# Kernel optimization log

Hardware: AMD Instinct MI355X
Metric: run time of the kernel (lower is better)

The kernel has to match this reference:

```python
import jax, jax.numpy as jnp
import numpy as np

N = 50000      # num nodes
E = 800000     # num edges (before self loops)
DIN = 128      # input_dim
HID = 32       # hidden_dim per head
HEADS = 4
DOUT = 128     # output_dim
NEG_SLOPE = 0.2
EPS = 1e-5


def setup_inputs() -> dict:
    key = jax.random.key(0)
    ks = jax.random.split(key, 16)
    s = 0.05
    return {
        "x": jax.random.normal(ks[0], (N, DIN), dtype=jnp.float32),
        "edge_index": jax.random.randint(ks[1], (2, E), 0, N, dtype=jnp.int64),
        # GAT layer 1 (heads=4, concat=True)
        "W1": jax.random.normal(ks[2], (DIN, HEADS * HID), dtype=jnp.float32) * s,
        "att_src1": jax.random.normal(ks[3], (HEADS, HID), dtype=jnp.float32) * s,
        "att_dst1": jax.random.normal(ks[4], (HEADS, HID), dtype=jnp.float32) * s,
        "b1": jnp.zeros((HEADS * HID,), dtype=jnp.float32),
        # GAT layer 2 (heads=1, concat=False)
        "W2": jax.random.normal(ks[5], (HEADS * HID, DOUT), dtype=jnp.float32) * s,
        "att_src2": jax.random.normal(ks[6], (1, DOUT), dtype=jnp.float32) * s,
        "att_dst2": jax.random.normal(ks[7], (1, DOUT), dtype=jnp.float32) * s,
        "b2": jnp.zeros((DOUT,), dtype=jnp.float32),
        # LayerNorms
        "g1": jnp.ones((HEADS * HID,), dtype=jnp.float32),
        "be1": jnp.zeros((HEADS * HID,), dtype=jnp.float32),
        "g2": jnp.ones((DOUT,), dtype=jnp.float32),
        "be2": jnp.zeros((DOUT,), dtype=jnp.float32),
    }


def gat_conv(x, src, dst, W, a_src, a_dst, n_nodes):
    # x: [N, Fin]; W: [Fin, H*C]; a_src/a_dst: [H, C]
    H, C = a_src.shape
    h = (x @ W).reshape(-1, H, C)                       # [N, H, C]
    es = jnp.einsum("nhc,hc->nh", h, a_src)             # [N, H]
    ed = jnp.einsum("nhc,hc->nh", h, a_dst)             # [N, H]
    e = jax.nn.leaky_relu(es[src] + ed[dst], NEG_SLOPE)  # [E, H]
    # segment softmax over incoming edges of each dst node
    m = jax.ops.segment_max(e, dst, num_segments=n_nodes)
    a = jnp.exp(e - jax.lax.stop_gradient(m)[dst])
    den = jax.ops.segment_sum(a, dst, num_segments=n_nodes)
    alpha = a / den[dst]                                 # [E, H]
    out = jax.ops.segment_sum(alpha[:, :, None] * h[src], dst,
                              num_segments=n_nodes)      # [N, H, C]
    return out


def layer_norm(x, g, b):
    mu = jnp.mean(x, axis=-1, keepdims=True)
    var = jnp.mean((x - mu) ** 2, axis=-1, keepdims=True)
    return (x - mu) * jax.lax.rsqrt(var + EPS) * g + b


def reference(x, edge_index, W1, att_src1, att_dst1, b1,
              W2, att_src2, att_dst2, b2, g1, be1, g2, be2):
    n = x.shape[0]
    loop = jnp.arange(n, dtype=edge_index.dtype)
    src = jnp.concatenate([edge_index[0], loop])  # PyG add_self_loops=True
    dst = jnp.concatenate([edge_index[1], loop])

    h = gat_conv(x, src, dst, W1, att_src1, att_dst1, n)   # [N, 4, 32]
    h = h.reshape(n, -1) + b1                              # concat=True
    h = jax.nn.relu(layer_norm(h, g1, be1))                # dropout = id (eval)

    o = gat_conv(h, src, dst, W2, att_src2, att_dst2, n)   # [N, 1, DOUT]
    o = o[:, 0, :] + b2                                    # concat=False, 1 head
    o = jax.nn.relu(layer_norm(o, g2, be2))
    return o
```

## Files before the change

kernel.cpp:

```cpp
#include <hip/hip_runtime.h>

#define NEG 0.2f
#define LNEPS 1e-5f

static __device__ __forceinline__ float leaky(float e){ return fmaxf(e, NEG*e); }

static __device__ __forceinline__ unsigned pack_bf16(float a, float b){
  unsigned ua = __float_as_uint(a), ub = __float_as_uint(b);
  ua += 0x7FFFu + ((ua>>16)&1u);
  ub += 0x7FFFu + ((ub>>16)&1u);
  return (ua>>16) | (ub & 0xFFFF0000u);
}
static __device__ __forceinline__ float lo_bf(unsigned u){ return __uint_as_float(u<<16); }
static __device__ __forceinline__ float hi_bf(unsigned u){ return __uint_as_float(u & 0xFFFF0000u); }

typedef float f32x4 __attribute__((ext_vector_type(4)));
typedef short s16x8 __attribute__((ext_vector_type(8)));
union U4V8 { uint4 u; s16x8 v; };


__global__ __launch_bounds__(256) void k_bhist(const int* __restrict__ dst, int* __restrict__ bcnt, int E){
  __shared__ int h[256];
  int t = threadIdx.x;
  h[t] = 0; __syncthreads();
  int base = blockIdx.x * 2048;
  int cnt = min(2048, E - base);
  for (int i = t; i < cnt; i += 256) atomicAdd(&h[((unsigned)dst[base+i]) >> 8], 1);
  __syncthreads();
  if (h[t]) atomicAdd(&bcnt[t], h[t]);
}

__global__ __launch_bounds__(256) void k_bscan(const int* __restrict__ bcnt, int* __restrict__ boff,
                                               int* __restrict__ off, int N, int E){
  __shared__ int sm[256];
  int t = threadIdx.x;
  int v = bcnt[t];
  sm[t] = v; __syncthreads();
  for (int o=1;o<256;o<<=1){ int add=(t>=o)?sm[t-o]:0; __syncthreads(); sm[t]+=add; __syncthreads(); }
  boff[t+1] = sm[t];
  if (t==0){ boff[0] = 0; off[N] = E; }
}

__global__ __launch_bounds__(256) void k_bstage(const int* __restrict__ src, const int* __restrict__ dst,
                                                const int* __restrict__ boff, int* __restrict__ bfill,
                                                unsigned* __restrict__ stage, int E){
  __shared__ int h[256];
  __shared__ int sm[256];
  __shared__ int sb[256];
  __shared__ int cur[256];
  __shared__ int rb[256];
  __shared__ unsigned buf[2048];
  int t = threadIdx.x;
  h[t] = 0; __syncthreads();
  int base = blockIdx.x * 2048;
  int cnt = min(2048, E - base);
  for (int i = t; i < cnt; i += 256) atomicAdd(&h[((unsigned)dst[base+i]) >> 8], 1);
  __syncthreads();
  int hv = h[t];
  sm[t] = hv; __syncthreads();
  for (int o=1;o<256;o<<=1){ int add=(t>=o)?sm[t-o]:0; __syncthreads(); sm[t]+=add; __syncthreads(); }
  sb[t] = sm[t] - hv;
  cur[t] = sm[t] - hv;
  rb[t] = (hv > 0) ? atomicAdd(&bfill[t], hv) : 0;
  __syncthreads();
  for (int i = t; i < cnt; i += 256){
    unsigned d = (unsigned)dst[base+i];
    unsigned v = (unsigned)src[base+i] | (d << 16);
    int p = atomicAdd(&cur[d >> 8], 1);
    buf[p] = v;
  }
  __syncthreads();
  for (int i = t; i < cnt; i += 256){
    unsigned v = buf[i];
    int b = v >> 24;
    stage[ (size_t)(boff[b] + rb[b] + (i - sb[b])) ] = v;
  }
}

__global__ __launch_bounds__(1024) void k_bucket(const unsigned* __restrict__ stage, const int* __restrict__ boff,
                                                 int* __restrict__ off, unsigned* __restrict__ csr2, int N){
  __shared__ int cnt[256];
  __shared__ int sm[256];
  __shared__ int cur[256];
  int b = blockIdx.x, t = threadIdx.x;
  int lo = boff[b], hi = boff[b+1];
  if (t < 256) cnt[t] = 0;
  __syncthreads();
  for (int i = lo + t; i < hi; i += 1024) atomicAdd(&cnt[(stage[i] >> 16) & 0xFF], 1);
  __syncthreads();
  if (t < 256){ sm[t] = cnt[t]; }
  __syncthreads();
  for (int o=1;o<256;o<<=1){
    int add = (t < 256 && t >= o) ? sm[t-o] : 0;
    __syncthreads();
    if (t < 256) sm[t] += add;
    __syncthreads();
  }
  if (t < 256){
    int ex = sm[t] - cnt[t];
    cur[t] = ex;
    int d = (b << 8) + t;
    if (d < N) off[d] = lo + ex;
  }
  __syncthreads();
  for (int i = lo + t; i < hi; i += 1024){
    unsigned v = stage[i];
    int p = atomicAdd(&cur[(v >> 16) & 0xFF], 1);
    csr2[(size_t)(lo + p)] = v;
  }
}


__global__ __launch_bounds__(256) void k_wprep(const float* __restrict__ W, uint4* __restrict__ Wb){
  int i = blockIdx.x*256 + threadIdx.x;
  int lane = i & 63, t = (i>>6)&7, k0 = i>>9;
  int c = lane & 15, q = lane >> 4;
  const float* base = &W[(size_t)(k0*32 + q*8)*128 + t*16 + c];
  uint4 u;
  u.x = pack_bf16(base[0*128], base[1*128]);
  u.y = pack_bf16(base[2*128], base[3*128]);
  u.z = pack_bf16(base[4*128], base[5*128]);
  u.w = pack_bf16(base[6*128], base[7*128]);
  Wb[i] = u;
}


template<int HEADS, bool PACKED>
__global__ __launch_bounds__(256) void k_gemm_mfma(const float* __restrict__ A,
                                                   const unsigned* __restrict__ Ab,
                                                   const uint4* __restrict__ Wb,
                                                   const float* __restrict__ as, const float* __restrict__ ad,
                                                   unsigned* __restrict__ Hb, float* __restrict__ es,
                                                   float* __restrict__ ed, float* __restrict__ m0, int n){
  __shared__ unsigned hstage[4][16*68];
  int tid = threadIdx.x;
  int wave = tid >> 6, lane = tid & 63;
  int c = lane & 15, q = lane >> 4;
  int r0 = blockIdx.x*64 + wave*16;
  int rowa = r0 + c;
  int rowc = min(rowa, n-1);
  f32x4 acc[8];
  #pragma unroll
  for (int t=0;t<8;++t) acc[t] = (f32x4){0.f,0.f,0.f,0.f};

  #pragma unroll
  for (int k0 = 0; k0 < 4; ++k0){
    U4V8 af;
    if (PACKED){
      af.u = *(const uint4*)&Ab[(size_t)rowc*64 + k0*16 + q*4];
    } else {
      const float* ap = &A[(size_t)rowc*128 + k0*32 + q*8];
      float4 v0 = *(const float4*)ap;
      float4 v1 = *(const float4*)(ap+4);
      af.u.x = pack_bf16(v0.x, v0.y);
      af.u.y = pack_bf16(v0.z, v0.w);
      af.u.z = pack_bf16(v1.x, v1.y);
      af.u.w = pack_bf16(v1.z, v1.w);
    }
    #pragma unroll
    for (int t=0;t<8;++t){
      U4V8 bf;
      bf.u = Wb[(k0*8+t)*64 + lane];
      acc[t] = __builtin_amdgcn_mfma_f32_16x16x32_bf16(af.v, bf.v, acc[t], 0, 0, 0);
    }
  }

  float asv[8], adv[8];
  #pragma unroll
  for (int t=0;t<8;++t){ asv[t] = as[t*16+c]; adv[t] = ad[t*16+c]; }
  if (HEADS == 4){
    float pes[4][4], ped[4][4];
    #pragma unroll
    for (int r=0;r<4;++r)
      #pragma unroll
      for (int h=0;h<4;++h){ pes[r][h]=0.f; ped[r][h]=0.f; }
    #pragma unroll
    for (int t=0;t<8;++t)
      #pragma unroll
      for (int r=0;r<4;++r){
        pes[r][t>>1] = fmaf(acc[t][r], asv[t], pes[r][t>>1]);
        ped[r][t>>1] = fmaf(acc[t][r], adv[t], ped[r][t>>1]);
      }
    #pragma unroll
    for (int r=0;r<4;++r)
      #pragma unroll
      for (int h=0;h<4;++h){
        #pragma unroll
        for (int m=1;m<16;m<<=1){
          pes[r][h] += __shfl_xor(pes[r][h], m);
          ped[r][h] += __shfl_xor(ped[r][h], m);
        }
      }
    if (c == 0){
      #pragma unroll
      for (int r=0;r<4;++r){
        int row2 = r0 + q*4 + r;
        if (row2 < n){
          float4 e = make_float4(pes[r][0],pes[r][1],pes[r][2],pes[r][3]);
          float4 d = make_float4(ped[r][0],ped[r][1],ped[r][2],ped[r][3]);
          float4 mm = make_float4(leaky(e.x+d.x),leaky(e.y+d.y),leaky(e.z+d.z),leaky(e.w+d.w));
          *(float4*)&es[(size_t)row2*4] = e;
          *(float4*)&ed[(size_t)row2*4] = d;
          *(float4*)&m0[(size_t)row2*4] = mm;
        }
      }
    }
  } else {
    float pes[4] = {0.f,0.f,0.f,0.f}, ped[4] = {0.f,0.f,0.f,0.f};
    #pragma unroll
    for (int t=0;t<8;++t)
      #pragma unroll
      for (int r=0;r<4;++r){
        pes[r] = fmaf(acc[t][r], asv[t], pes[r]);
        ped[r] = fmaf(acc[t][r], adv[t], ped[r]);
      }
    #pragma unroll
    for (int r=0;r<4;++r){
      #pragma unroll
      for (int m=1;m<16;m<<=1){
        pes[r] += __shfl_xor(pes[r], m);
        ped[r] += __shfl_xor(ped[r], m);
      }
    }
    if (c == 0){
      #pragma unroll
      for (int r=0;r<4;++r){
        int row2 = r0 + q*4 + r;
        if (row2 < n){
          es[row2] = pes[r]; ed[row2] = ped[r]; m0[row2] = leaky(pes[r]+ped[r]);
        }
      }
    }
  }

  unsigned* hs = hstage[wave];
  #pragma unroll
  for (int t=0;t<8;++t)
    #pragma unroll
    for (int r=0;r<4;++r){
      float other = __shfl_xor(acc[t][r], 1);
      if (!(c & 1)) hs[(q*4+r)*68 + t*8 + (c>>1)] = pack_bf16(acc[t][r], other);
    }
  #pragma unroll
  for (int it=0; it<4; ++it){
    int idx = it*64 + lane;
    int rr = idx >> 4, c4 = idx & 15;
    int grow = r0 + rr;
    if (grow < n)
      *(uint4*)&Hb[(size_t)grow*64 + c4*4] = *(uint4*)&hs[rr*68 + c4*4];
  }
}


template<bool OUT_PACKED>
__global__ __launch_bounds__(256) void k_agg4(const unsigned* __restrict__ Hb,
                                              const float* __restrict__ es, const float* __restrict__ ed,
                                              const float* __restrict__ m0,
                                              const int* __restrict__ off, const unsigned* __restrict__ csr2,
                                              const float* __restrict__ bias, const float* __restrict__ g,
                                              const float* __restrict__ be, float* __restrict__ out,
                                              unsigned* __restrict__ outp, int N){
  int lane = threadIdx.x & 63;
  int node = blockIdx.x*4 + (threadIdx.x >> 6);
  if (node >= N) return;
  int hh = lane >> 4;
  int wsrc = lane & 48;
  float edn = ed[(size_t)node*4 + hh];
  float m0n = m0[(size_t)node*4 + hh];
  float l = 1.f;
  unsigned uself = Hb[(size_t)node*64 + lane];
  float a1 = lo_bf(uself), a2 = hi_bf(uself);
  int j0 = off[node], j1 = off[node+1];
  for (int c0 = j0; c0 < j1; c0 += 16){
    int m = min(16, j1 - c0);
    int eidx = lane & 15;
    int sv = 0; float wv = 0.f;
    if (eidx < m){
      unsigned v = csr2[c0 + eidx];
      sv = v & 0xFFFF;
      float e = es[(size_t)sv*4 + hh];
      wv = __expf(leaky(e + edn) - m0n);
    }
    int j = 0;
    for (; j+3 < m; j += 4){
      int s0 = __shfl(sv, j), s1 = __shfl(sv, j+1), s2 = __shfl(sv, j+2), s3 = __shfl(sv, j+3);
      float w0 = __shfl(wv, wsrc | j);
      float w1 = __shfl(wv, wsrc | (j+1));
      float w2 = __shfl(wv, wsrc | (j+2));
      float w3 = __shfl(wv, wsrc | (j+3));
      unsigned u0 = Hb[(size_t)s0*64 + lane];
      unsigned u1 = Hb[(size_t)s1*64 + lane];
      unsigned u2 = Hb[(size_t)s2*64 + lane];
      unsigned u3 = Hb[(size_t)s3*64 + lane];
      l += (w0 + w1) + (w2 + w3);
      a1 = fmaf(w0, lo_bf(u0), a1); a2 = fmaf(w0, hi_bf(u0), a2);
      a1 = fmaf(w1, lo_bf(u1), a1); a2 = fmaf(w1, hi_bf(u1), a2);
      a1 = fmaf(w2, lo_bf(u2), a1); a2 = fmaf(w2, hi_bf(u2), a2);
      a1 = fmaf(w3, lo_bf(u3), a1); a2 = fmaf(w3, hi_bf(u3), a2);
    }
    for (; j < m; ++j){
      int s0 = __shfl(sv, j);
      float w0 = __shfl(wv, wsrc | j);
      unsigned u0 = Hb[(size_t)s0*64 + lane];
      l += w0;
      a1 = fmaf(w0, lo_bf(u0), a1); a2 = fmaf(w0, hi_bf(u0), a2);
    }
  }
  float rl = __frcp_rn(l);
  float2 bv = *(const float2*)&bias[2*lane];
  float v1 = a1 * rl + bv.x;
  float v2 = a2 * rl + bv.y;
  float s = v1 + v2;
  #pragma unroll
  for (int m=32;m>0;m>>=1) s += __shfl_xor(s,m);
  float mu = s * (1.f/128.f);
  float d1 = v1-mu, d2 = v2-mu;
  float ss = d1*d1 + d2*d2;
  #pragma unroll
  for (int m=32;m>0;m>>=1) ss += __shfl_xor(ss,m);
  float rs = rsqrtf(ss*(1.f/128.f) + LNEPS);
  float2 gv = *(const float2*)&g[2*lane];
  float2 bev = *(const float2*)&be[2*lane];
  float y1 = fmaxf(d1*rs*gv.x + bev.x, 0.f);
  float y2 = fmaxf(d2*rs*gv.y + bev.y, 0.f);
  if (OUT_PACKED){
    outp[(size_t)node*64 + lane] = pack_bf16(y1, y2);
  } else {
    *(float2*)&out[(size_t)node*128 + 2*lane] = make_float2(y1, y2);
  }
}

__global__ __launch_bounds__(256) void k_agg1(const unsigned* __restrict__ Hb,
                                              const float* __restrict__ es, const float* __restrict__ ed,
                                              const float* __restrict__ m0,
                                              const int* __restrict__ off, const unsigned* __restrict__ csr2,
                                              const float* __restrict__ bias, const float* __restrict__ g,
                                              const float* __restrict__ be, float* __restrict__ out, int N){
  int lane = threadIdx.x & 63;
  int node = blockIdx.x*4 + (threadIdx.x >> 6);
  if (node >= N) return;
  float edn = ed[node];
  float m0n = m0[node];
  float l = 1.f;
  unsigned uself = Hb[(size_t)node*64 + lane];
  float a1 = lo_bf(uself), a2 = hi_bf(uself);
  int j0 = off[node], j1 = off[node+1];
  for (int c0 = j0; c0 < j1; c0 += 64){
    int m = min(64, j1 - c0);
    int sv = 0; float wv = 0.f;
    if (lane < m){
      unsigned v = csr2[c0 + lane];
      sv = v & 0xFFFF;
      wv = __expf(leaky(es[sv] + edn) - m0n);
    }
    int j = 0;
    for (; j+3 < m; j += 4){
      int s0 = __shfl(sv, j), s1 = __shfl(sv, j+1), s2 = __shfl(sv, j+2), s3 = __shfl(sv, j+3);
      float w0 = __shfl(wv, j), w1 = __shfl(wv, j+1), w2 = __shfl(wv, j+2), w3 = __shfl(wv, j+3);
      unsigned u0 = Hb[(size_t)s0*64 + lane];
      unsigned u1 = Hb[(size_t)s1*64 + lane];
      unsigned u2 = Hb[(size_t)s2*64 + lane];
      unsigned u3 = Hb[(size_t)s3*64 + lane];
      l += (w0 + w1) + (w2 + w3);
      a1 = fmaf(w0, lo_bf(u0), a1); a2 = fmaf(w0, hi_bf(u0), a2);
      a1 = fmaf(w1, lo_bf(u1), a1); a2 = fmaf(w1, hi_bf(u1), a2);
      a1 = fmaf(w2, lo_bf(u2), a1); a2 = fmaf(w2, hi_bf(u2), a2);
      a1 = fmaf(w3, lo_bf(u3), a1); a2 = fmaf(w3, hi_bf(u3), a2);
    }
    for (; j < m; ++j){
      int s0 = __shfl(sv, j);
      float w0 = __shfl(wv, j);
      unsigned u0 = Hb[(size_t)s0*64 + lane];
      l += w0;
      a1 = fmaf(w0, lo_bf(u0), a1); a2 = fmaf(w0, hi_bf(u0), a2);
    }
  }
  float rl = __frcp_rn(l);
  float2 bv = *(const float2*)&bias[2*lane];
  float v1 = a1 * rl + bv.x;
  float v2 = a2 * rl + bv.y;
  float s = v1 + v2;
  #pragma unroll
  for (int mm=32;mm>0;mm>>=1) s += __shfl_xor(s,mm);
  float mu = s * (1.f/128.f);
  float d1 = v1-mu, d2 = v2-mu;
  float ss = d1*d1 + d2*d2;
  #pragma unroll
  for (int mm=32;mm>0;mm>>=1) ss += __shfl_xor(ss,mm);
  float rs = rsqrtf(ss*(1.f/128.f) + LNEPS);
  float2 gv = *(const float2*)&g[2*lane];
  float2 bev = *(const float2*)&be[2*lane];
  float y1 = fmaxf(d1*rs*gv.x + bev.x, 0.f);
  float y2 = fmaxf(d2*rs*gv.y + bev.y, 0.f);
  *(float2*)&out[(size_t)node*128 + 2*lane] = make_float2(y1, y2);
}


extern "C" void kernel_launch(void* const* d_in, const int* in_sizes, int n_in,
                              void* d_out, int out_size, void* d_ws, size_t ws_size,
                              hipStream_t stream){
  const float* x   = (const float*)d_in[0];
  const int*   ei  = (const int*)  d_in[1];
  const float* W1  = (const float*)d_in[2];
  const float* as1 = (const float*)d_in[3];
  const float* ad1 = (const float*)d_in[4];
  const float* b1  = (const float*)d_in[5];
  const float* W2  = (const float*)d_in[6];
  const float* as2 = (const float*)d_in[7];
  const float* ad2 = (const float*)d_in[8];
  const float* b2  = (const float*)d_in[9];
  const float* g1  = (const float*)d_in[10];
  const float* be1 = (const float*)d_in[11];
  const float* g2  = (const float*)d_in[12];
  const float* be2 = (const float*)d_in[13];

  int N = in_sizes[0] / 128;
  int E = in_sizes[1] / 2;
  const int* src = ei;
  const int* dst = ei + E;

  char* p = (char*)d_ws;
  auto carve = [&](size_t bytes)->char*{ char* r = p; p += ((bytes + 255) / 256) * 256; return r; };
  unsigned* Hb = (unsigned*)carve((size_t)N*64*4);
  unsigned* Bb = (unsigned*)carve((size_t)N*64*4);
  float* es1 = (float*)carve((size_t)N*4*4);
  float* ed1 = (float*)carve((size_t)N*4*4);
  float* m01 = (float*)carve((size_t)N*4*4);
  float* es2 = (float*)carve((size_t)N*4);
  float* ed2 = (float*)carve((size_t)N*4);
  float* m02 = (float*)carve((size_t)N*4);
  int* off   = (int*)carve((size_t)(N+1)*4);
  unsigned* stg = (unsigned*)carve((size_t)E*4);
  unsigned* csr2= (unsigned*)carve((size_t)E*4);
  uint4* W1b = (uint4*)carve(2048*16);
  uint4* W2b = (uint4*)carve(2048*16);
  int* bcnt  = (int*)carve(256*4);
  int* bfill = (int*)carve(256*4);
  int* boff  = (int*)carve(257*4);

  hipMemsetAsync(bcnt, 0, 256*4, stream);
  hipMemsetAsync(bfill, 0, 256*4, stream);

  int nbe = (E + 2047) / 2048;
  int NB  = (N + 255) >> 8;
  int gb  = (N + 63) / 64;
  int nb4 = (N + 3) / 4;

  k_wprep <<<8, 256, 0, stream>>>(W1, W1b);
  k_wprep <<<8, 256, 0, stream>>>(W2, W2b);
  k_bhist <<<nbe, 256, 0, stream>>>(dst, bcnt, E);
  k_bscan <<<1,   256, 0, stream>>>(bcnt, boff, off, N, E);
  k_bstage<<<nbe, 256, 0, stream>>>(src, dst, boff, bfill, stg, E);
  k_bucket<<<NB, 1024, 0, stream>>>(stg, boff, off, csr2, N);

  k_gemm_mfma<4,false><<<gb, 256, 0, stream>>>(x, nullptr, W1b, as1, ad1, Hb, es1, ed1, m01, N);
  k_agg4<true><<<nb4, 256, 0, stream>>>(Hb, es1, ed1, m01, off, csr2, b1, g1, be1, nullptr, Bb, N);
  k_gemm_mfma<1,true><<<gb, 256, 0, stream>>>(nullptr, Bb, W2b, as2, ad2, Hb, es2, ed2, m02, N);
  k_agg1<<<nb4, 256, 0, stream>>>(Hb, es2, ed2, m02, off, csr2, b2, g2, be2, (float*)d_out, N);
}
```

Measured before the change: 255.0 us.

## Use wave-level scans, merge prep launches and memsets, unroll gathers by eight

Replaces the 256-element barrier-based Hillis-Steele scans in the CSR build kernels with a single-wave shuffle scan. Merges the two weight-prep launches into one and the two counter memsets into one covering both adjacent buffers. Adds an 8-way unrolled gather loop in both aggregation kernels so more independent row loads are in flight. The goal is fewer launches and barriers plus more memory-level parallelism, at the cost of higher register pressure in the aggregation kernels. The merged memset depends on the two counter buffers being laid out back to back.

After: 247.4 us. 1.03x faster.

```diff
diff --git a/kernel.cpp b/kernel.cpp
--- a/kernel.cpp
+++ b/kernel.cpp
@@ -17,6 +17,20 @@
 typedef float f32x4 __attribute__((ext_vector_type(4)));
 typedef short s16x8 __attribute__((ext_vector_type(8)));
 union U4V8 { uint4 u; s16x8 v; };
+
+static __device__ __forceinline__ void wave_scan256(int* sm, int t){
+  if (t < 64){
+    int a0=sm[t*4], a1=sm[t*4+1], a2=sm[t*4+2], a3=sm[t*4+3];
+    int s = a0+a1+a2+a3, sc = s;
+    #pragma unroll
+    for (int o=1;o<64;o<<=1){ int x = __shfl_up(sc, o); if (t >= o) sc += x; }
+    int e = sc - s;
+    sm[t*4]   = e;
+    sm[t*4+1] = e + a0;
+    sm[t*4+2] = e + a0 + a1;
+    sm[t*4+3] = e + a0 + a1 + a2;
+  }
+}
 
 
 __global__ __launch_bounds__(256) void k_bhist(const int* __restrict__ dst, int* __restrict__ bcnt, int E){
@@ -36,8 +50,9 @@
   int t = threadIdx.x;
   int v = bcnt[t];
   sm[t] = v; __syncthreads();
-  for (int o=1;o<256;o<<=1){ int add=(t>=o)?sm[t-o]:0; __syncthreads(); sm[t]+=add; __syncthreads(); }
-  boff[t+1] = sm[t];
+  wave_scan256(sm, t);
+  __syncthreads();
+  boff[t+1] = sm[t] + v;
   if (t==0){ boff[0] = 0; off[N] = E; }
 }
 
@@ -58,9 +73,11 @@
   __syncthreads();
   int hv = h[t];
   sm[t] = hv; __syncthreads();
-  for (int o=1;o<256;o<<=1){ int add=(t>=o)?sm[t-o]:0; __syncthreads(); sm[t]+=add; __syncthreads(); }
-  sb[t] = sm[t] - hv;
-  cur[t] = sm[t] - hv;
+  wave_scan256(sm, t);
+  __syncthreads();
+  int excl = sm[t];
+  sb[t] = excl;
+  cur[t] = excl;
   rb[t] = (hv > 0) ? atomicAdd(&bfill[t], hv) : 0;
   __syncthreads();
   for (int i = t; i < cnt; i += 256){
@@ -88,16 +105,12 @@
   __syncthreads();
   for (int i = lo + t; i < hi; i += 1024) atomicAdd(&cnt[(stage[i] >> 16) & 0xFF], 1);
   __syncthreads();
-  if (t < 256){ sm[t] = cnt[t]; }
-  __syncthreads();
-  for (int o=1;o<256;o<<=1){
-    int add = (t < 256 && t >= o) ? sm[t-o] : 0;
-    __syncthreads();
-    if (t < 256) sm[t] += add;
-    __syncthreads();
-  }
+  if (t < 256) sm[t] = cnt[t];
+  __syncthreads();
+  wave_scan256(sm, t);
+  __syncthreads();
   if (t < 256){
-    int ex = sm[t] - cnt[t];
+    int ex = sm[t];
     cur[t] = ex;
     int d = (b << 8) + t;
     if (d < N) off[d] = lo + ex;
@@ -111,9 +124,13 @@
 }
 
 
-__global__ __launch_bounds__(256) void k_wprep(const float* __restrict__ W, uint4* __restrict__ Wb){
+__global__ __launch_bounds__(256) void k_wprep(const float* __restrict__ W1, const float* __restrict__ W2,
+                                               uint4* __restrict__ W1b, uint4* __restrict__ W2b){
   int i = blockIdx.x*256 + threadIdx.x;
-  int lane = i & 63, t = (i>>6)&7, k0 = i>>9;
+  const float* W = (i < 2048) ? W1 : W2;
+  uint4* Wb = (i < 2048) ? W1b : W2b;
+  int ii = i & 2047;
+  int lane = ii & 63, t = (ii>>6)&7, k0 = ii>>9;
   int c = lane & 15, q = lane >> 4;
   const float* base = &W[(size_t)(k0*32 + q*8)*128 + t*16 + c];
   uint4 u;
@@ -121,7 +138,7 @@
   u.y = pack_bf16(base[2*128], base[3*128]);
   u.z = pack_bf16(base[4*128], base[5*128]);
   u.w = pack_bf16(base[6*128], base[7*128]);
-  Wb[i] = u;
+  Wb[ii] = u;
 }
 
 
@@ -278,16 +295,38 @@
     if (eidx < m){
       unsigned v = csr2[c0 + eidx];
       sv = v & 0xFFFF;
-      float e = es[(size_t)sv*4 + hh];
-      wv = __expf(leaky(e + edn) - m0n);
+      wv = __expf(leaky(es[(size_t)sv*4 + hh] + edn) - m0n);
     }
     int j = 0;
+    for (; j+7 < m; j += 8){
+      int s0 = __shfl(sv, j),   s1 = __shfl(sv, j+1), s2 = __shfl(sv, j+2), s3 = __shfl(sv, j+3);
+      int s4 = __shfl(sv, j+4), s5 = __shfl(sv, j+5), s6 = __shfl(sv, j+6), s7 = __shfl(sv, j+7);
+      float w0 = __shfl(wv, wsrc | j),     w1 = __shfl(wv, wsrc | (j+1));
+      float w2 = __shfl(wv, wsrc | (j+2)), w3 = __shfl(wv, wsrc | (j+3));
+      float w4 = __shfl(wv, wsrc | (j+4)), w5 = __shfl(wv, wsrc | (j+5));
+      float w6 = __shfl(wv, wsrc | (j+6)), w7 = __shfl(wv, wsrc | (j+7));
+      unsigned u0 = Hb[(size_t)s0*64 + lane];
+      unsigned u1 = Hb[(size_t)s1*64 + lane];
+      unsigned u2 = Hb[(size_t)s2*64 + lane];
+      unsigned u3 = Hb[(size_t)s3*64 + lane];
+      unsigned u4 = Hb[(size_t)s4*64 + lane];
+      unsigned u5 = Hb[(size_t)s5*64 + lane];
+      unsigned u6 = Hb[(size_t)s6*64 + lane];
+      unsigned u7 = Hb[(size_t)s7*64 + lane];
+      l += ((w0 + w1) + (w2 + w3)) + ((w4 + w5) + (w6 + w7));
+      a1 = fmaf(w0, lo_bf(u0), a1); a2 = fmaf(w0, hi_bf(u0), a2);
+      a1 = fmaf(w1, lo_bf(u1), a1); a2 = fmaf(w1, hi_bf(u1), a2);
+      a1 = fmaf(w2, lo_bf(u2), a1); a2 = fmaf(w2, hi_bf(u2), a2);
+      a1 = fmaf(w3, lo_bf(u3), a1); a2 = fmaf(w3, hi_bf(u3), a2);
+      a1 = fmaf(w4, lo_bf(u4), a1); a2 = fmaf(w4, hi_bf(u4), a2);
+      a1 = fmaf(w5, lo_bf(u5), a1); a2 = fmaf(w5, hi_bf(u5), a2);
+      a1 = fmaf(w6, lo_bf(u6), a1); a2 = fmaf(w6, hi_bf(u6), a2);
+      a1 = fmaf(w7, lo_bf(u7), a1); a2 = fmaf(w7, hi_bf(u7), a2);
+    }
     for (; j+3 < m; j += 4){
       int s0 = __shfl(sv, j), s1 = __shfl(sv, j+1), s2 = __shfl(sv, j+2), s3 = __shfl(sv, j+3);
-      float w0 = __shfl(wv, wsrc | j);
-      float w1 = __shfl(wv, wsrc | (j+1));
-      float w2 = __shfl(wv, wsrc | (j+2));
-      float w3 = __shfl(wv, wsrc | (j+3));
+      float w0 = __shfl(wv, wsrc | j),     w1 = __shfl(wv, wsrc | (j+1));
+      float w2 = __shfl(wv, wsrc | (j+2)), w3 = __shfl(wv, wsrc | (j+3));
       unsigned u0 = Hb[(size_t)s0*64 + lane];
       unsigned u1 = Hb[(size_t)s1*64 + lane];
       unsigned u2 = Hb[(size_t)s2*64 + lane];
@@ -354,6 +393,29 @@
       wv = __expf(leaky(es[sv] + edn) - m0n);
     }
     int j = 0;
+    for (; j+7 < m; j += 8){
+      int s0 = __shfl(sv, j),   s1 = __shfl(sv, j+1), s2 = __shfl(sv, j+2), s3 = __shfl(sv, j+3);
+      int s4 = __shfl(sv, j+4), s5 = __shfl(sv, j+5), s6 = __shfl(sv, j+6), s7 = __shfl(sv, j+7);
+      float w0 = __shfl(wv, j),   w1 = __shfl(wv, j+1), w2 = __shfl(wv, j+2), w3 = __shfl(wv, j+3);
+      float w4 = __shfl(wv, j+4), w5 = __shfl(wv, j+5), w6 = __shfl(wv, j+6), w7 = __shfl(wv, j+7);
+      unsigned u0 = Hb[(size_t)s0*64 + lane];
+      unsigned u1 = Hb[(size_t)s1*64 + lane];
+      unsigned u2 = Hb[(size_t)s2*64 + lane];
+      unsigned u3 = Hb[(size_t)s3*64 + lane];
+      unsigned u4 = Hb[(size_t)s4*64 + lane];
+      unsigned u5 = Hb[(size_t)s5*64 + lane];
+      unsigned u6 = Hb[(size_t)s6*64 + lane];
+      unsigned u7 = Hb[(size_t)s7*64 + lane];
+      l += ((w0 + w1) + (w2 + w3)) + ((w4 + w5) + (w6 + w7));
+      a1 = fmaf(w0, lo_bf(u0), a1); a2 = fmaf(w0, hi_bf(u0), a2);
+      a1 = fmaf(w1, lo_bf(u1), a1); a2 = fmaf(w1, hi_bf(u1), a2);
+      a1 = fmaf(w2, lo_bf(u2), a1); a2 = fmaf(w2, hi_bf(u2), a2);
+      a1 = fmaf(w3, lo_bf(u3), a1); a2 = fmaf(w3, hi_bf(u3), a2);
+      a1 = fmaf(w4, lo_bf(u4), a1); a2 = fmaf(w4, hi_bf(u4), a2);
+      a1 = fmaf(w5, lo_bf(u5), a1); a2 = fmaf(w5, hi_bf(u5), a2);
+      a1 = fmaf(w6, lo_bf(u6), a1); a2 = fmaf(w6, hi_bf(u6), a2);
+      a1 = fmaf(w7, lo_bf(u7), a1); a2 = fmaf(w7, hi_bf(u7), a2);
+    }
     for (; j+3 < m; j += 4){
       int s0 = __shfl(sv, j), s1 = __shfl(sv, j+1), s2 = __shfl(sv, j+2), s3 = __shfl(sv, j+3);
       float w0 = __shfl(wv, j), w1 = __shfl(wv, j+1), w2 = __shfl(wv, j+2), w3 = __shfl(wv, j+3);
@@ -438,16 +500,14 @@
   int* bfill = (int*)carve(256*4);
   int* boff  = (int*)carve(257*4);
 
-  hipMemsetAsync(bcnt, 0, 256*4, stream);
-  hipMemsetAsync(bfill, 0, 256*4, stream);
+  hipMemsetAsync(bcnt, 0, 2048, stream);
 
   int nbe = (E + 2047) / 2048;
   int NB  = (N + 255) >> 8;
   int gb  = (N + 63) / 64;
   int nb4 = (N + 3) / 4;
 
-  k_wprep <<<8, 256, 0, stream>>>(W1, W1b);
-  k_wprep <<<8, 256, 0, stream>>>(W2, W2b);
+  k_wprep <<<16, 256, 0, stream>>>(W1, W2, W1b, W2b);
   k_bhist <<<nbe, 256, 0, stream>>>(dst, bcnt, E);
   k_bscan <<<1,   256, 0, stream>>>(bcnt, boff, off, N, E);
   k_bstage<<<nbe, 256, 0, stream>>>(src, dst, boff, bfill, stg, E);
```
